# Kernel optimization log

Measured on AMD Instinct MI355X. Metric: run time of the kernel, lower is better.

Reference implementation:

```python
import jax, jax.numpy as jnp
import numpy as np

TOP_K = 2
EPS = float(np.finfo(np.float64).eps)  # combine() clamps zeros to np.finfo(float).eps


def setup_inputs() -> dict:
    key = jax.random.key(0)
    ks = jax.random.split(key, 6)
    B, D, H, O, E = 2048, 1024, 2048, 512, 8
    return {
        "x": jax.random.normal(ks[0], (B, D), dtype=jnp.float32),
        "w_gate": jax.random.normal(ks[1], (D, E), dtype=jnp.float32) * 0.02,
        "fc1_w": jax.random.normal(ks[2], (E, D, H), dtype=jnp.float32) * 0.02,
        "fc1_b": jax.random.normal(ks[3], (E, H), dtype=jnp.float32) * 0.02,
        "fc2_w": jax.random.normal(ks[4], (E, H, O), dtype=jnp.float32) * 0.02,
        "fc2_b": jax.random.normal(ks[5], (E, O), dtype=jnp.float32) * 0.02,
    }


def _gates(x, w_gate):
    # Noisy top-k gating in eval mode (no noise): clean logits -> top-k -> softmax over top-k -> scatter.
    logits = x @ w_gate                              # [B, E]
    top_logits, top_idx = jax.lax.top_k(logits, TOP_K)  # [B, K]
    top_gates = jax.nn.softmax(top_logits, axis=-1)      # 'softmax' gating over selected experts
    B = x.shape[0]
    gates = jnp.zeros(logits.shape, logits.dtype)
    gates = gates.at[jnp.arange(B)[:, None], top_idx].set(top_gates)
    return gates                                      # [B, E], zero for non-selected experts


def reference(x, w_gate, fc1_w, fc1_b, fc2_w, fc2_b):
    gates = _gates(x, w_gate)                         # [B, E]
    # Dense-equivalent of SparseDispatcher: non-selected experts have gate 0,
    # so weighting by gates reproduces dispatch/expert/combine exactly.
    h = jax.nn.gelu(jnp.einsum('bd,edh->ebh', x, fc1_w) + fc1_b[:, None, :],
                    approximate=False)                # [E, B, H]
    logp = jax.nn.log_softmax(jnp.einsum('ebh,eho->ebo', h, fc2_w) + fc2_b[:, None, :],
                              axis=-1)                # [E, B, O] (MLP ends with LogSoftmax)
    # combine: sum_e gates[b,e] * exp(logp_e[b]), clamp zeros to eps, then log
    combined = jnp.einsum('ebo,be->bo', jnp.exp(logp), gates)  # [B, O]
    combined = jnp.where(combined == 0, jnp.asarray(EPS, combined.dtype), combined)
    return jnp.log(combined)
```

## Files before the change

### kernel.cpp

```cpp
#include <hip/hip_runtime.h>
#include <stdint.h>

#define Bn 2048
#define Dn 1024
#define Hn 2048
#define On 512
#define En 8

typedef float f32x4 __attribute__((ext_vector_type(4)));
typedef unsigned short ushort_t;
typedef unsigned char u8;

__device__ __forceinline__ void gload16(const void* g, void* l) {
  __builtin_amdgcn_global_load_lds((const uint32_t*)g, (uint32_t*)l, 16, 0, 0);
}

__device__ __forceinline__ int pk4_fp8(float a, float b, float c, float d) {
  int w = __builtin_amdgcn_cvt_pk_fp8_f32(a, b, 0, false);
  w = __builtin_amdgcn_cvt_pk_fp8_f32(c, d, w, true);
  return w;
}

__device__ __forceinline__ u8 f2fp8(float v) {
  int w = __builtin_amdgcn_cvt_pk_fp8_f32(v, v, 0, false);
  return (u8)(w & 0xff);
}

__global__ void init_kernel(int* counts, int* cursors) {
  int t = threadIdx.x;
  if (t < En) { counts[t] = 0; cursors[t] = 0; }
}

#define NB_G (Bn / 8)
#define NB_T1 ((Dn / 256) * (Hn / 64) * En)
#define NB_T2 ((Hn / 256) * (On / 64) * En)
#define NB_X (Bn * Dn / 4096)
#define WSCALE 64.0f

__device__ __forceinline__ void tcast_f8_256(const float* __restrict__ inp,
                                             u8* __restrict__ outp,
                                             int R, int C, int r0, int c0, u8* lds) {
  int t = threadIdx.x;
  int cc4 = (t & 15) * 4;
  int rr4 = (t >> 4) * 4;
#pragma unroll
  for (int pass = 0; pass < 4; pass++) {
    int rbase = pass * 64 + rr4;
    uint32_t wds[4] = {0, 0, 0, 0};
#pragma unroll
    for (int i = 0; i < 4; i++) {
      float4 v = *(const float4*)&inp[(size_t)(r0 + rbase + i) * C + c0 + cc4];
      wds[0] |= (uint32_t)f2fp8(v.x * WSCALE) << (8 * i);
      wds[1] |= (uint32_t)f2fp8(v.y * WSCALE) << (8 * i);
      wds[2] |= (uint32_t)f2fp8(v.z * WSCALE) << (8 * i);
      wds[3] |= (uint32_t)f2fp8(v.w * WSCALE) << (8 * i);
    }
#pragma unroll
    for (int j = 0; j < 4; j++)
      *(uint32_t*)&lds[(cc4 + j) * 272 + rbase] = wds[j];
  }
  __syncthreads();
  int j = t >> 2, q = t & 3;
  const u8* lp = &lds[j * 272 + q * 64];
  int4 d0 = *(const int4*)(lp);
  int4 d1 = *(const int4*)(lp + 16);
  int4 d2 = *(const int4*)(lp + 32);
  int4 d3 = *(const int4*)(lp + 48);
  u8* op = &outp[(size_t)(c0 + j) * R + r0 + q * 64];
  *(int4*)(op) = d0;
  *(int4*)(op + 16) = d1;
  *(int4*)(op + 32) = d2;
  *(int4*)(op + 48) = d3;
}

__global__ __launch_bounds__(256) void prep_kernel(
    const float* __restrict__ x, const float* __restrict__ wg,
    const float* __restrict__ fc1w, const float* __restrict__ fc2w,
    u8* __restrict__ x_f8, u8* __restrict__ w1t8, u8* __restrict__ w2t8,
    int* __restrict__ top_idx, float* __restrict__ gates, int* __restrict__ counts) {
  __shared__ float smem[En * Dn];
  __shared__ int lcnt[En];
  int bid = blockIdx.x;
  int t = threadIdx.x;

  if (bid < NB_G) {
    float* wgs = smem;
    for (int i = t; i < Dn * En; i += 256) {
      int d = i >> 3, e = i & 7;
      wgs[e * Dn + d] = wg[i];
    }
    if (t < En) lcnt[t] = 0;
    __syncthreads();
    int w = t >> 6, lane = t & 63;
#pragma unroll
    for (int r = 0; r < 2; r++) {
      int b = bid * 8 + w * 2 + r;
      const float* xr = x + (size_t)b * Dn;
      float xv[16];
#pragma unroll
      for (int j = 0; j < 16; j++) xv[j] = xr[lane + j * 64];
      float acc[En];
#pragma unroll
      for (int e = 0; e < En; e++) acc[e] = 0.f;
#pragma unroll
      for (int j = 0; j < 16; j++) {
        int d = lane + j * 64;
#pragma unroll
        for (int e = 0; e < En; e++) acc[e] += xv[j] * wgs[e * Dn + d];
      }
#pragma unroll
      for (int off = 32; off; off >>= 1) {
#pragma unroll
        for (int e = 0; e < En; e++) acc[e] += __shfl_down(acc[e], off);
      }
      if (lane == 0) {
        float best = -1e30f, second = -1e30f; int bi = 0, si = 0;
#pragma unroll
        for (int e = 0; e < En; e++) {
          float l = acc[e];
          if (l > best) { second = best; si = bi; best = l; bi = e; }
          else if (l > second) { second = l; si = e; }
        }
        float e1 = expf(second - best);
        float inv = 1.f / (1.f + e1);
        top_idx[2 * b] = bi; top_idx[2 * b + 1] = si;
        gates[2 * b] = inv;  gates[2 * b + 1] = e1 * inv;
        atomicAdd(&lcnt[bi], 1);
        atomicAdd(&lcnt[si], 1);
      }
    }
    __syncthreads();
    if (t < En) {
      int c = lcnt[t];
      if (c) atomicAdd(&counts[t], c);
    }
  } else if (bid < NB_G + NB_T1) {
    int idx = bid - NB_G;
    constexpr int TPE = (Dn / 256) * (Hn / 64);
    int z = idx / TPE, rem = idx % TPE;
    int r0 = (rem / (Hn / 64)) * 256, c0 = (rem % (Hn / 64)) * 64;
    tcast_f8_256(fc1w + (size_t)z * Dn * Hn, w1t8 + (size_t)z * Dn * Hn, Dn, Hn, r0, c0,
                 (u8*)smem);
  } else if (bid < NB_G + NB_T1 + NB_T2) {
    int idx = bid - NB_G - NB_T1;
    constexpr int TPE = (Hn / 256) * (On / 64);
    int z = idx / TPE, rem = idx % TPE;
    int r0 = (rem / (On / 64)) * 256, c0 = (rem % (On / 64)) * 64;
    tcast_f8_256(fc2w + (size_t)z * Hn * On, w2t8 + (size_t)z * Hn * On, Hn, On, r0, c0,
                 (u8*)smem);
  } else {
    int i = (bid - NB_G - NB_T1 - NB_T2) * 256 + t;
    const float4* p = (const float4*)x + (size_t)i * 4;
    float4 a = p[0], b = p[1], c = p[2], d = p[3];
    int4 o;
    o.x = pk4_fp8(a.x, a.y, a.z, a.w);
    o.y = pk4_fp8(b.x, b.y, b.z, b.w);
    o.z = pk4_fp8(c.x, c.y, c.z, c.w);
    o.w = pk4_fp8(d.x, d.y, d.z, d.w);
    *(int4*)(x_f8 + (size_t)i * 16) = o;
  }
}

__global__ void offsets_kernel(const int* counts, int* offsets, int* cursors) {
  if (threadIdx.x == 0) {
    int s = 0;
    for (int e = 0; e < En; e++) { offsets[e] = s; s += counts[e]; }
  }
  if (threadIdx.x < En) cursors[threadIdx.x] = 0;
}

__global__ void assign_kernel(const int* __restrict__ top_idx, const int* __restrict__ offsets,
                              int* cursors, int* __restrict__ s2r, int* __restrict__ r2s) {
  int b = blockIdx.x * 256 + threadIdx.x;
  if (b >= Bn) return;
#pragma unroll
  for (int k = 0; k < 2; k++) {
    int e = top_idx[2 * b + k];
    int pos = atomicAdd(&cursors[e], 1);
    int slot = offsets[e] + pos;
    s2r[slot] = b;
    r2s[2 * b + k] = slot;
  }
}

template <bool FC1, int N, int K, int SPLITK>
__global__ __launch_bounds__(256, 8) void fp8_gemm_kernel(
    const u8* __restrict__ A, const u8* __restrict__ WT,
    const float* __restrict__ bias, const int* __restrict__ offsets,
    const int* __restrict__ counts, const int* __restrict__ s2r,
    u8* __restrict__ outH8, float* __restrict__ outL, float* __restrict__ outL2) {
  constexpr int NBL = N / 64;
  constexpr int KS = K / SPLITK;
  constexpr int NT = KS / 64;
  int e = blockIdx.z;
  int cnt = counts[e];
  int rb = blockIdx.y;
  if (rb * 64 >= cnt) return;
  int base = offsets[e];
  int ks = blockIdx.x / NBL;
  int nb = (blockIdx.x % NBL) * 64;
  int k0 = ks * KS;
  __shared__ __align__(16) u8 As[64 * 64];
  __shared__ __align__(16) u8 Bs[64 * 64];
  int t = threadIdx.x;
  int lane = t & 63, w = t >> 6;
  int wr = w >> 1, wc = w & 1;

  int srow = t >> 2;
  int sslot = (t & 3) ^ ((srow >> 1) & 3);
  int scol = sslot * 16;

  int lr = rb * 64 + srow;
  int lrc = lr < cnt ? lr : cnt - 1;
  const u8* aptr = A + (size_t)(FC1 ? s2r[base + lrc] : (base + lrc)) * K + k0 + scol;
  const u8* bptr = WT + ((size_t)e * N + nb + srow) * K + k0 + scol;

  f32x4 zero = {0.f, 0.f, 0.f, 0.f};
  f32x4 acc[2][2];
#pragma unroll
  for (int m = 0; m < 2; m++)
#pragma unroll
    for (int n = 0; n < 2; n++) acc[m][n] = zero;

  int a_r = wr * 32 + (lane & 15);
  int b_r = wc * 32 + (lane & 15);
  int rkey = ((lane & 15) >> 1) & 3;
  int slb = (lane >> 4) >> 1;
  int half = ((lane >> 4) & 1) * 8;

  for (int kt = 0; kt < NT; kt++) {
    gload16(aptr + kt * 64, &As[t * 16]);
    gload16(bptr + kt * 64, &Bs[t * 16]);
    __syncthreads();
#pragma unroll
    for (int kk = 0; kk < 2; kk++) {
      long af[2], bfr[2];
#pragma unroll
      for (int m = 0; m < 2; m++)
        af[m] = *(const long*)(As + (a_r + m * 16) * 64 +
                               (((kk * 2 + slb) ^ rkey) << 4) + half);
#pragma unroll
      for (int n = 0; n < 2; n++)
        bfr[n] = *(const long*)(Bs + (b_r + n * 16) * 64 +
                                (((kk * 2 + slb) ^ rkey) << 4) + half);
#pragma unroll
      for (int m = 0; m < 2; m++)
#pragma unroll
        for (int n = 0; n < 2; n++)
          acc[m][n] = __builtin_amdgcn_mfma_f32_16x16x32_fp8_fp8(af[m], bfr[n], acc[m][n], 0, 0, 0);
    }
    __syncthreads();
  }

  const float INV = 1.0f / WSCALE;
  float* dst = (SPLITK > 1 && ks > 0) ? outL2 : outL;
  int lr0 = rb * 64 + wr * 32;
#pragma unroll
  for (int m = 0; m < 2; m++) {
#pragma unroll
    for (int i = 0; i < 4; i++) {
      int orow = lr0 + m * 16 + (lane >> 4) * 4 + i;
      if (orow < cnt) {
        int slot = base + orow;
#pragma unroll
        for (int n = 0; n < 2; n++) {
          int col = nb + wc * 32 + n * 16 + (lane & 15);
          if (FC1) {
            float v = acc[m][n][i] * INV + bias[e * N + col];
            float g = 0.5f * v * (1.0f + erff(v * 0.70710678118654752f));
            outH8[(size_t)slot * N + col] = f2fp8(g);
          } else {
            float v = acc[m][n][i] * INV + (ks == 0 ? bias[e * N + col] : 0.f);
            dst[(size_t)slot * N + col] = v;
          }
        }
      }
    }
  }
}

__device__ __forceinline__ float blk_reduce(float v, bool ismax) {
  __shared__ float sbuf[4];
  int lane = threadIdx.x & 63, w = threadIdx.x >> 6;
#pragma unroll
  for (int off = 32; off; off >>= 1) {
    float o = __shfl_down(v, off);
    v = ismax ? fmaxf(v, o) : (v + o);
  }
  __syncthreads();
  if (lane == 0) sbuf[w] = v;
  __syncthreads();
  float r = sbuf[0];
#pragma unroll
  for (int i = 1; i < 4; i++) r = ismax ? fmaxf(r, sbuf[i]) : (r + sbuf[i]);
  return r;
}

__global__ void combine_kernel(const float* __restrict__ l2a, const float* __restrict__ l2b,
                               const int* __restrict__ r2s, const float* __restrict__ gates,
                               float* __restrict__ out) {
  int b = blockIdx.x, t = threadIdx.x;
  float c0 = 0.f, c1 = 0.f;
#pragma unroll
  for (int k = 0; k < 2; k++) {
    int slot = r2s[2 * b + k];
    float g = gates[2 * b + k];
    const float* lp0 = l2a + (size_t)slot * On;
    const float* lp1 = l2b + (size_t)slot * On;
    float v0 = lp0[t] + lp1[t];
    float v1 = lp0[t + 256] + lp1[t + 256];
    float m = blk_reduce(fmaxf(v0, v1), true);
    float s = blk_reduce(expf(v0 - m) + expf(v1 - m), false);
    float lse = m + logf(s);
    c0 += g * expf(v0 - lse);
    c1 += g * expf(v1 - lse);
  }
  const float EPSv = 2.220446049250313e-16f;
  out[(size_t)b * On + t] = logf(fmaxf(c0, EPSv));
  out[(size_t)b * On + t + 256] = logf(fmaxf(c1, EPSv));
}

extern "C" void kernel_launch(void* const* d_in, const int* in_sizes, int n_in,
                              void* d_out, int out_size, void* d_ws, size_t ws_size,
                              hipStream_t stream) {
  const float* x = (const float*)d_in[0];
  const float* wgate = (const float*)d_in[1];
  const float* fc1w = (const float*)d_in[2];
  const float* fc1b = (const float*)d_in[3];
  const float* fc2w = (const float*)d_in[4];
  const float* fc2b = (const float*)d_in[5];
  float* out = (float*)d_out;

  char* ws = (char*)d_ws;
  size_t o = 0;
  u8* x_f8     = (u8*)(ws + o);    o += (size_t)Bn * Dn;
  u8* w1t8     = (u8*)(ws + o);    o += (size_t)En * Hn * Dn;
  u8* w2t8     = (u8*)(ws + o);    o += (size_t)En * On * Hn;
  u8* hbuf8    = (u8*)(ws + o);    o += (size_t)2 * Bn * Hn;
  float* l2buf = (float*)(ws + o); o += (size_t)2 * Bn * On * 4;
  int* top_idx = (int*)(ws + o);   o += (size_t)Bn * 2 * 4;
  float* gates = (float*)(ws + o); o += (size_t)Bn * 2 * 4;
  int* r2s     = (int*)(ws + o);   o += (size_t)Bn * 2 * 4;
  int* s2r     = (int*)(ws + o);   o += (size_t)2 * Bn * 4;
  int* counts  = (int*)(ws + o);   o += 64;
  int* offsets = (int*)(ws + o);   o += 64;
  int* cursors = (int*)(ws + o);   o += 64;
  float* l2buf1 = (float*)w1t8;

  hipLaunchKernelGGL(init_kernel, dim3(1), dim3(64), 0, stream, counts, cursors);
  hipLaunchKernelGGL(prep_kernel, dim3(NB_G + NB_T1 + NB_T2 + NB_X), dim3(256), 0, stream,
                     x, wgate, fc1w, fc2w, x_f8, w1t8, w2t8, top_idx, gates, counts);
  hipLaunchKernelGGL(offsets_kernel, dim3(1), dim3(64), 0, stream, counts, offsets, cursors);
  hipLaunchKernelGGL(assign_kernel, dim3(Bn / 256), dim3(256), 0, stream,
                     top_idx, offsets, cursors, s2r, r2s);
  hipLaunchKernelGGL((fp8_gemm_kernel<true, Hn, Dn, 1>), dim3(Hn / 64, 32, En), dim3(256),
                     0, stream, x_f8, w1t8, fc1b, offsets, counts, s2r, hbuf8,
                     (float*)nullptr, (float*)nullptr);
  hipLaunchKernelGGL((fp8_gemm_kernel<false, On, Hn, 2>), dim3((On / 64) * 2, 32, En), dim3(256),
                     0, stream, hbuf8, w2t8, fc2b, offsets, counts, s2r, (u8*)nullptr,
                     l2buf, l2buf1);
  hipLaunchKernelGGL(combine_kernel, dim3(Bn), dim3(256), 0, stream, l2buf, l2buf1, r2s, gates, out);
}
```

Baseline: 115.6 us.

## Fuse x fp8 cast into gating, drop offsets kernel, pad transpose LDS

The gating blocks now handle one row per wave and write the fp8 copy of x while reading it, which removes the separate x-cast block range and a second read of x. The offsets kernel is removed: assign_kernel and the GEMM kernels compute expert prefix offsets inline from counts, saving one launch. The weight transpose-cast uses a dword-indexed LDS buffer with a stride of 65 dwords to avoid bank conflicts. The x cast now uses scalar byte stores instead of packed 16-byte stores, which may cost write efficiency. The cursors are no longer reset between prep and assign, but init_kernel already zeroes them.

```diff
diff --git a/kernel.cpp b/kernel.cpp
--- a/kernel.cpp
+++ b/kernel.cpp
@@ -8,17 +8,10 @@
 #define En 8
 
 typedef float f32x4 __attribute__((ext_vector_type(4)));
-typedef unsigned short ushort_t;
 typedef unsigned char u8;
 
 __device__ __forceinline__ void gload16(const void* g, void* l) {
   __builtin_amdgcn_global_load_lds((const uint32_t*)g, (uint32_t*)l, 16, 0, 0);
-}
-
-__device__ __forceinline__ int pk4_fp8(float a, float b, float c, float d) {
-  int w = __builtin_amdgcn_cvt_pk_fp8_f32(a, b, 0, false);
-  w = __builtin_amdgcn_cvt_pk_fp8_f32(c, d, w, true);
-  return w;
 }
 
 __device__ __forceinline__ u8 f2fp8(float v) {
@@ -31,21 +24,20 @@
   if (t < En) { counts[t] = 0; cursors[t] = 0; }
 }
 
-#define NB_G (Bn / 8)
+#define NB_G (Bn / 4)
 #define NB_T1 ((Dn / 256) * (Hn / 64) * En)
 #define NB_T2 ((Hn / 256) * (On / 64) * En)
-#define NB_X (Bn * Dn / 4096)
 #define WSCALE 64.0f
 
 __device__ __forceinline__ void tcast_f8_256(const float* __restrict__ inp,
                                              u8* __restrict__ outp,
-                                             int R, int C, int r0, int c0, u8* lds) {
+                                             int R, int C, int r0, int c0, uint32_t* L) {
   int t = threadIdx.x;
   int cc4 = (t & 15) * 4;
-  int rr4 = (t >> 4) * 4;
-#pragma unroll
-  for (int pass = 0; pass < 4; pass++) {
-    int rbase = pass * 64 + rr4;
+  int rg = t >> 4;
+#pragma unroll
+  for (int p = 0; p < 4; p++) {
+    int rbase = p * 64 + rg * 4;
     uint32_t wds[4] = {0, 0, 0, 0};
 #pragma unroll
     for (int i = 0; i < 4; i++) {
@@ -55,22 +47,22 @@
       wds[2] |= (uint32_t)f2fp8(v.z * WSCALE) << (8 * i);
       wds[3] |= (uint32_t)f2fp8(v.w * WSCALE) << (8 * i);
     }
-#pragma unroll
-    for (int j = 0; j < 4; j++)
-      *(uint32_t*)&lds[(cc4 + j) * 272 + rbase] = wds[j];
+    int rd = p * 16 + rg;
+#pragma unroll
+    for (int j = 0; j < 4; j++) L[(cc4 + j) * 65 + rd] = wds[j];
   }
   __syncthreads();
-  int j = t >> 2, q = t & 3;
-  const u8* lp = &lds[j * 272 + q * 64];
-  int4 d0 = *(const int4*)(lp);
-  int4 d1 = *(const int4*)(lp + 16);
-  int4 d2 = *(const int4*)(lp + 32);
-  int4 d3 = *(const int4*)(lp + 48);
-  u8* op = &outp[(size_t)(c0 + j) * R + r0 + q * 64];
-  *(int4*)(op) = d0;
-  *(int4*)(op + 16) = d1;
-  *(int4*)(op + 32) = d2;
-  *(int4*)(op + 48) = d3;
+  int c = t >> 2, q = t & 3;
+  uint32_t dw[16];
+#pragma unroll
+  for (int i = 0; i < 16; i++) dw[i] = L[c * 65 + q * 16 + i];
+  u8* op = &outp[(size_t)(c0 + c) * R + r0 + q * 64];
+#pragma unroll
+  for (int s = 0; s < 4; s++) {
+    int4 o = make_int4((int)dw[4 * s], (int)dw[4 * s + 1], (int)dw[4 * s + 2],
+                       (int)dw[4 * s + 3]);
+    *(int4*)(op + 16 * s) = o;
+  }
 }
 
 __global__ __launch_bounds__(256) void prep_kernel(
@@ -78,7 +70,7 @@
     const float* __restrict__ fc1w, const float* __restrict__ fc2w,
     u8* __restrict__ x_f8, u8* __restrict__ w1t8, u8* __restrict__ w2t8,
     int* __restrict__ top_idx, float* __restrict__ gates, int* __restrict__ counts) {
-  __shared__ float smem[En * Dn];
+  __shared__ __align__(16) float smem[En * Dn];
   __shared__ int lcnt[En];
   int bid = blockIdx.x;
   int t = threadIdx.x;
@@ -92,42 +84,41 @@
     if (t < En) lcnt[t] = 0;
     __syncthreads();
     int w = t >> 6, lane = t & 63;
-#pragma unroll
-    for (int r = 0; r < 2; r++) {
-      int b = bid * 8 + w * 2 + r;
-      const float* xr = x + (size_t)b * Dn;
-      float xv[16];
-#pragma unroll
-      for (int j = 0; j < 16; j++) xv[j] = xr[lane + j * 64];
-      float acc[En];
-#pragma unroll
-      for (int e = 0; e < En; e++) acc[e] = 0.f;
-#pragma unroll
-      for (int j = 0; j < 16; j++) {
-        int d = lane + j * 64;
-#pragma unroll
-        for (int e = 0; e < En; e++) acc[e] += xv[j] * wgs[e * Dn + d];
+    int b = bid * 4 + w;
+    const float* xr = x + (size_t)b * Dn;
+    u8* xo = x_f8 + (size_t)b * Dn;
+    float xv[16];
+#pragma unroll
+    for (int j = 0; j < 16; j++) xv[j] = xr[lane + j * 64];
+    float acc[En];
+#pragma unroll
+    for (int e = 0; e < En; e++) acc[e] = 0.f;
+#pragma unroll
+    for (int j = 0; j < 16; j++) {
+      int d = lane + j * 64;
+      xo[d] = f2fp8(xv[j]);
+#pragma unroll
+      for (int e = 0; e < En; e++) acc[e] += xv[j] * wgs[e * Dn + d];
+    }
+#pragma unroll
+    for (int off = 32; off; off >>= 1) {
+#pragma unroll
+      for (int e = 0; e < En; e++) acc[e] += __shfl_down(acc[e], off);
+    }
+    if (lane == 0) {
+      float best = -1e30f, second = -1e30f; int bi = 0, si = 0;
+#pragma unroll
+      for (int e = 0; e < En; e++) {
+        float l = acc[e];
+        if (l > best) { second = best; si = bi; best = l; bi = e; }
+        else if (l > second) { second = l; si = e; }
       }
-#pragma unroll
-      for (int off = 32; off; off >>= 1) {
-#pragma unroll
-        for (int e = 0; e < En; e++) acc[e] += __shfl_down(acc[e], off);
-      }
-      if (lane == 0) {
-        float best = -1e30f, second = -1e30f; int bi = 0, si = 0;
-#pragma unroll
-        for (int e = 0; e < En; e++) {
-          float l = acc[e];
-          if (l > best) { second = best; si = bi; best = l; bi = e; }
-          else if (l > second) { second = l; si = e; }
-        }
-        float e1 = expf(second - best);
-        float inv = 1.f / (1.f + e1);
-        top_idx[2 * b] = bi; top_idx[2 * b + 1] = si;
-        gates[2 * b] = inv;  gates[2 * b + 1] = e1 * inv;
-        atomicAdd(&lcnt[bi], 1);
-        atomicAdd(&lcnt[si], 1);
-      }
+      float e1 = expf(second - best);
+      float inv = 1.f / (1.f + e1);
+      top_idx[2 * b] = bi; top_idx[2 * b + 1] = si;
+      gates[2 * b] = inv;  gates[2 * b + 1] = e1 * inv;
+      atomicAdd(&lcnt[bi], 1);
+      atomicAdd(&lcnt[si], 1);
     }
     __syncthreads();
     if (t < En) {
@@ -140,44 +131,30 @@
     int z = idx / TPE, rem = idx % TPE;
     int r0 = (rem / (Hn / 64)) * 256, c0 = (rem % (Hn / 64)) * 64;
     tcast_f8_256(fc1w + (size_t)z * Dn * Hn, w1t8 + (size_t)z * Dn * Hn, Dn, Hn, r0, c0,
-                 (u8*)smem);
-  } else if (bid < NB_G + NB_T1 + NB_T2) {
+                 (uint32_t*)smem);
+  } else {
     int idx = bid - NB_G - NB_T1;
     constexpr int TPE = (Hn / 256) * (On / 64);
     int z = idx / TPE, rem = idx % TPE;
     int r0 = (rem / (On / 64)) * 256, c0 = (rem % (On / 64)) * 64;
     tcast_f8_256(fc2w + (size_t)z * Hn * On, w2t8 + (size_t)z * Hn * On, Hn, On, r0, c0,
-                 (u8*)smem);
-  } else {
-    int i = (bid - NB_G - NB_T1 - NB_T2) * 256 + t;
-    const float4* p = (const float4*)x + (size_t)i * 4;
-    float4 a = p[0], b = p[1], c = p[2], d = p[3];
-    int4 o;
-    o.x = pk4_fp8(a.x, a.y, a.z, a.w);
-    o.y = pk4_fp8(b.x, b.y, b.z, b.w);
-    o.z = pk4_fp8(c.x, c.y, c.z, c.w);
-    o.w = pk4_fp8(d.x, d.y, d.z, d.w);
-    *(int4*)(x_f8 + (size_t)i * 16) = o;
-  }
-}
-
-__global__ void offsets_kernel(const int* counts, int* offsets, int* cursors) {
-  if (threadIdx.x == 0) {
-    int s = 0;
-    for (int e = 0; e < En; e++) { offsets[e] = s; s += counts[e]; }
-  }
-  if (threadIdx.x < En) cursors[threadIdx.x] = 0;
-}
-
-__global__ void assign_kernel(const int* __restrict__ top_idx, const int* __restrict__ offsets,
+                 (uint32_t*)smem);
+  }
+}
+
+__global__ void assign_kernel(const int* __restrict__ top_idx, const int* __restrict__ counts,
                               int* cursors, int* __restrict__ s2r, int* __restrict__ r2s) {
   int b = blockIdx.x * 256 + threadIdx.x;
   if (b >= Bn) return;
+  int offs[En];
+  int s = 0;
+#pragma unroll
+  for (int e = 0; e < En; e++) { offs[e] = s; s += counts[e]; }
 #pragma unroll
   for (int k = 0; k < 2; k++) {
     int e = top_idx[2 * b + k];
     int pos = atomicAdd(&cursors[e], 1);
-    int slot = offsets[e] + pos;
+    int slot = offs[e] + pos;
     s2r[slot] = b;
     r2s[2 * b + k] = slot;
   }
@@ -186,8 +163,8 @@
 template <bool FC1, int N, int K, int SPLITK>
 __global__ __launch_bounds__(256, 8) void fp8_gemm_kernel(
     const u8* __restrict__ A, const u8* __restrict__ WT,
-    const float* __restrict__ bias, const int* __restrict__ offsets,
-    const int* __restrict__ counts, const int* __restrict__ s2r,
+    const float* __restrict__ bias, const int* __restrict__ counts,
+    const int* __restrict__ s2r,
     u8* __restrict__ outH8, float* __restrict__ outL, float* __restrict__ outL2) {
   constexpr int NBL = N / 64;
   constexpr int KS = K / SPLITK;
@@ -196,7 +173,9 @@
   int cnt = counts[e];
   int rb = blockIdx.y;
   if (rb * 64 >= cnt) return;
-  int base = offsets[e];
+  int base = 0;
+#pragma unroll
+  for (int i = 0; i < En; i++) base += (i < e) ? counts[i] : 0;
   int ks = blockIdx.x / NBL;
   int nb = (blockIdx.x % NBL) * 64;
   int k0 = ks * KS;
@@ -343,21 +322,19 @@
   int* r2s     = (int*)(ws + o);   o += (size_t)Bn * 2 * 4;
   int* s2r     = (int*)(ws + o);   o += (size_t)2 * Bn * 4;
   int* counts  = (int*)(ws + o);   o += 64;
-  int* offsets = (int*)(ws + o);   o += 64;
   int* cursors = (int*)(ws + o);   o += 64;
   float* l2buf1 = (float*)w1t8;
 
   hipLaunchKernelGGL(init_kernel, dim3(1), dim3(64), 0, stream, counts, cursors);
-  hipLaunchKernelGGL(prep_kernel, dim3(NB_G + NB_T1 + NB_T2 + NB_X), dim3(256), 0, stream,
+  hipLaunchKernelGGL(prep_kernel, dim3(NB_G + NB_T1 + NB_T2), dim3(256), 0, stream,
                      x, wgate, fc1w, fc2w, x_f8, w1t8, w2t8, top_idx, gates, counts);
-  hipLaunchKernelGGL(offsets_kernel, dim3(1), dim3(64), 0, stream, counts, offsets, cursors);
   hipLaunchKernelGGL(assign_kernel, dim3(Bn / 256), dim3(256), 0, stream,
-                     top_idx, offsets, cursors, s2r, r2s);
+                     top_idx, counts, cursors, s2r, r2s);
   hipLaunchKernelGGL((fp8_gemm_kernel<true, Hn, Dn, 1>), dim3(Hn / 64, 32, En), dim3(256),
-                     0, stream, x_f8, w1t8, fc1b, offsets, counts, s2r, hbuf8,
+                     0, stream, x_f8, w1t8, fc1b, counts, s2r, hbuf8,
                      (float*)nullptr, (float*)nullptr);
   hipLaunchKernelGGL((fp8_gemm_kernel<false, On, Hn, 2>), dim3((On / 64) * 2, 32, En), dim3(256),
-                     0, stream, hbuf8, w2t8, fc2b, offsets, counts, s2r, (u8*)nullptr,
+                     0, stream, hbuf8, w2t8, fc2b, counts, s2r, (u8*)nullptr,
                      l2buf, l2buf1);
   hipLaunchKernelGGL(combine_kernel, dim3(Bn), dim3(256), 0, stream, l2buf, l2buf1, r2s, gates, out);
 }
```

Measured after the change: 114.0 us. About the same (-1.4%).
